# Kernel tuning notes

Hardware: AMD Instinct MI355X
Metric: run time of the kernel (lower is better)

## Reference

```python
import jax, jax.numpy as jnp
import numpy as np

N, E, D, H, L = 100000, 800000, 64, 2, 2
C = D  # out_channels per head
NEG_SLOPE = 0.2


def setup_inputs() -> dict:
    key = jax.random.key(0)
    ks = jax.random.split(key, 10)
    x = jax.random.normal(ks[0], (N, D), dtype=jnp.float32)
    # random edges with no self loops (PyG GATv2 removes then re-adds self loops)
    src = jax.random.randint(ks[1], (E,), 0, N, dtype=jnp.int64)
    off = jax.random.randint(ks[2], (E,), 1, N, dtype=jnp.int64)
    dst = (src + off) % N
    edges_connectivity = jnp.stack([src, dst], axis=0)
    s = 1.0 / np.sqrt(D)
    Wl = jax.random.normal(ks[3], (L, D, H * C), dtype=jnp.float32) * s
    bl = jnp.zeros((L, H * C), dtype=jnp.float32)
    Wr = jax.random.normal(ks[4], (L, D, H * C), dtype=jnp.float32) * s
    br = jnp.zeros((L, H * C), dtype=jnp.float32)
    att = jax.random.normal(ks[5], (L, H, C), dtype=jnp.float32) * s
    bias = jnp.zeros((L, C), dtype=jnp.float32)
    return {"embeded_nodes_features": x, "edges_connectivity": edges_connectivity,
            "Wl": Wl, "bl": bl, "Wr": Wr, "br": br, "att": att, "bias": bias}


def _gatv2_layer(x, src, dst, Wl, bl, Wr, br, att, bias):
    # x: [N, D]; src/dst: [E'] (self loops already appended)
    xl = (x @ Wl + bl).reshape(N, H, C)
    xr = (x @ Wr + br).reshape(N, H, C)
    z = xl[src] + xr[dst]                                  # [E', H, C]
    e = jnp.einsum('ehc,hc->eh', jax.nn.leaky_relu(z, NEG_SLOPE), att)
    m = jax.ops.segment_max(e, dst, num_segments=N)        # [N, H]
    a = jnp.exp(e - m[dst])
    denom = jax.ops.segment_sum(a, dst, num_segments=N)    # [N, H]
    alpha = a / (denom[dst] + 1e-16)
    out = jax.ops.segment_sum(alpha[:, :, None] * xl[src], dst, num_segments=N)
    return out.mean(axis=1) + bias                         # concat=False -> mean over heads


def reference(embeded_nodes_features, edges_connectivity, Wl, bl, Wr, br, att, bias):
    loop = jnp.arange(N, dtype=edges_connectivity.dtype)
    src = jnp.concatenate([edges_connectivity[0], loop])
    dst = jnp.concatenate([edges_connectivity[1], loop])
    x = embeded_nodes_features  # dropout p=0 -> no-op
    for i in range(L):
        x = _gatv2_layer(x, src, dst, Wl[i], bl[i], Wr[i], br[i], att[i], bias[i])
        if i < L - 1:
            x = jax.nn.gelu(x)
    return x
```

## Files before the change

kernel.cpp:

```cpp
#include <hip/hip_runtime.h>
#include <math.h>

#define N_NODES 100000
#define N_EDGES 800000
#define D_IN    64
#define HC      128
#define CAP     48

#define GEMM_BLOCKS 1563
#define FUSED_BLOCKS (3 * GEMM_BLOCKS)

typedef short bf16x8 __attribute__((ext_vector_type(8)));
typedef float f32x4  __attribute__((ext_vector_type(4)));

__device__ __forceinline__ float gelu_f(float x) {
    float x3 = x * x * x;
    float y  = 0.7978845608028654f * (x + 0.044715f * x3);
    float t = 1.0f - 2.0f / (__expf(2.0f * y) + 1.0f);
    return 0.5f * x * (1.0f + t);
}

__device__ __forceinline__ float red16(float x) {
    x += __int_as_float(__builtin_amdgcn_mov_dpp(__float_as_int(x), 0x128, 0xF, 0xF, true));
    x += __int_as_float(__builtin_amdgcn_mov_dpp(__float_as_int(x), 0x124, 0xF, 0xF, true));
    x += __int_as_float(__builtin_amdgcn_mov_dpp(__float_as_int(x), 0x122, 0xF, 0xF, true));
    x += __int_as_float(__builtin_amdgcn_mov_dpp(__float_as_int(x), 0x121, 0xF, 0xF, true));
    return x;
}

__device__ __forceinline__ void bf16split(float x, unsigned short& h, unsigned short& l) {
    unsigned b  = __float_as_uint(x);
    unsigned hb = (b + 0x7FFFu + ((b >> 16) & 1u)) & 0xFFFF0000u;
    h = (unsigned short)(hb >> 16);
    float lo = x - __uint_as_float(hb);
    unsigned c = __float_as_uint(lo);
    l = (unsigned short)((c + 0x7FFFu + ((c >> 16) & 1u)) >> 16);
}

__global__ __launch_bounds__(256) void wprep_kernel(
    const float* __restrict__ Wl, const float* __restrict__ Wr,
    unsigned short* __restrict__ WBh, unsigned short* __restrict__ WBlo) {
    int g = blockIdx.x * 256 + threadIdx.x;
    int layer = g >> 14;
    int rem   = g & 16383;
    int j    = rem & 7;
    int idx  = rem >> 3;
    int lane = idx & 63;
    int kh   = (idx >> 6) & 1;
    int nt   = (idx >> 7) & 3;
    int w    = (idx >> 9) & 3;
    int col  = w * 64 + nt * 16 + (lane & 15);
    int k    = kh * 32 + (lane >> 4) * 8 + j;
    const float* W = (col < 128) ? Wl : Wr;
    float x = W[layer * 8192 + k * HC + (col & 127)];
    unsigned short h, l;
    bf16split(x, h, l);
    WBh[g] = h; WBlo[g] = l;
}

__global__ __launch_bounds__(256, 4) void gemm_scatter_kernel(
    const float* __restrict__ X,
    const unsigned short* __restrict__ WBh, const unsigned short* __restrict__ WBlo,
    const float* __restrict__ bl, const float* __restrict__ br,
    float* __restrict__ XL, float* __restrict__ XR,
    const int* __restrict__ edges, int* __restrict__ cnt, int* __restrict__ tbl,
    int fused) {
    __shared__ union SMem {
        struct { unsigned short XH[64 * 64]; unsigned short XLo[64 * 64]; } st;
        float CS[32 * 268];
    } sm;

    const int t = threadIdx.x;
    int gid;
    if (fused) {
        const int g = blockIdx.x / 3, r = blockIdx.x % 3;
        if (r != 2) {
            const int e = (2 * g + r) * 256 + t;
            if (e < N_EDGES) {
                int s = edges[e];
                int d = edges[N_EDGES + e];
                int slot = atomicAdd(&cnt[d], 1);
                if (slot < CAP) tbl[d * CAP + slot] = s;
            }
            return;
        }
        gid = g;
    } else {
        gid = blockIdx.x;
    }
    const int n0 = gid * 64;

    #pragma unroll
    for (int p = 0; p < 4; ++p) {
        int f   = p * 256 + t;
        int row = f >> 4, q = f & 15;
        int gn  = n0 + row;
        float4 v = make_float4(0.0f, 0.0f, 0.0f, 0.0f);
        if (gn < N_NODES) v = *(const float4*)(X + (size_t)gn * D_IN + 4 * q);
        ushort4 h, l;
        bf16split(v.x, h.x, l.x); bf16split(v.y, h.y, l.y);
        bf16split(v.z, h.z, l.z); bf16split(v.w, h.w, l.w);
        int off = row * 64 + ((((q >> 1) ^ (row & 7))) << 3) + ((q & 1) << 2);
        *(ushort4*)&sm.st.XH[off]  = h;
        *(ushort4*)&sm.st.XLo[off] = l;
    }
    __syncthreads();

    const int lane = t & 63;
    const int w    = __builtin_amdgcn_readfirstlane(t >> 6);
    const float* __restrict__ bp = (w < 2) ? bl : br;
    const int cbase = (w & 1) * 64;
    const int lc    = lane & 15;
    const int lq    = lane >> 4;

    f32x4 acc[4][4];
    #pragma unroll
    for (int nt = 0; nt < 4; ++nt) {
        float bv = bp[cbase + nt * 16 + lc];
        #pragma unroll
        for (int mt = 0; mt < 4; ++mt)
            acc[mt][nt] = (f32x4){bv, bv, bv, bv};
    }

    #pragma unroll
    for (int kh = 0; kh < 2; ++kh) {
        bf16x8 Bh[4], Bl[4];
        #pragma unroll
        for (int nt = 0; nt < 4; ++nt) {
            int a = (((w * 4 + nt) * 2 + kh) * 64 + lane) * 8;
            Bh[nt] = *(const bf16x8*)(WBh + a);
            Bl[nt] = *(const bf16x8*)(WBlo + a);
        }
        #pragma unroll
        for (int mt = 0; mt < 4; ++mt) {
            int row = mt * 16 + lc;
            int aoff = row * 64 + ((((kh << 2) + lq) ^ (row & 7)) << 3);
            bf16x8 Ah = *(const bf16x8*)(sm.st.XH + aoff);
            bf16x8 Al = *(const bf16x8*)(sm.st.XLo + aoff);
            #pragma unroll
            for (int nt = 0; nt < 4; ++nt)
                acc[mt][nt] = __builtin_amdgcn_mfma_f32_16x16x32_bf16(Ah, Bh[nt], acc[mt][nt], 0, 0, 0);
            #pragma unroll
            for (int nt = 0; nt < 4; ++nt)
                acc[mt][nt] = __builtin_amdgcn_mfma_f32_16x16x32_bf16(Al, Bh[nt], acc[mt][nt], 0, 0, 0);
            #pragma unroll
            for (int nt = 0; nt < 4; ++nt)
                acc[mt][nt] = __builtin_amdgcn_mfma_f32_16x16x32_bf16(Ah, Bl[nt], acc[mt][nt], 0, 0, 0);
        }
    }

    #pragma unroll
    for (int c = 0; c < 2; ++c) {
        __syncthreads();
        #pragma unroll
        for (int mt2 = 0; mt2 < 2; ++mt2) {
            int mt = 2 * c + mt2;
            #pragma unroll
            for (int nt = 0; nt < 4; ++nt)
                #pragma unroll
                for (int r = 0; r < 4; ++r)
                    sm.CS[(mt2 * 16 + (lq << 2) + r) * 268 + w * 64 + nt * 16 + lc]
                        = acc[mt][nt][r];
        }
        __syncthreads();
        #pragma unroll
        for (int i = 0; i < 8; ++i) {
            int lr = i * 4 + w;
            int n  = n0 + c * 32 + lr;
            if (n < N_NODES) {
                float4 v4 = *(const float4*)&sm.CS[lr * 268 + 4 * lane];
                float* o = ((lane < 32) ? XL : XR) + (size_t)n * HC + (lane & 31) * 4;
                *(float4*)o = v4;
            }
        }
    }
}

__global__ __launch_bounds__(256) void aggregate_kernel(
    const float* __restrict__ XL, const float* __restrict__ XR,
    const int* __restrict__ cnt, const int* __restrict__ tbl,
    const float* __restrict__ att, const float* __restrict__ bias,
    float* __restrict__ Y, int applyGelu) {
    const int wv   = (blockIdx.x * blockDim.x + threadIdx.x) >> 6;
    const int lane = threadIdx.x & 63;
    const int v    = 2 * wv + (lane >> 5);
    if (v >= N_NODES) return;
    const int li = lane & 15;
    const int hc = ((lane >> 4) & 1) * 64 + 4 * li;
    const int selbase = lane & 32;

    const float4 araw = *(const float4*)(att + hc);
    float4 a06, a04;
    a06.x = araw.x * 0.865617024f; a06.y = araw.y * 0.865617024f;
    a06.z = araw.z * 0.865617024f; a06.w = araw.w * 0.865617024f;
    a04.x = araw.x * 0.577078016f; a04.y = araw.y * 0.577078016f;
    a04.z = araw.z * 0.577078016f; a04.w = araw.w * 0.577078016f;
    const float4 xr4 = *(const float4*)(XR + (size_t)v * HC + hc);
    const float4 xl4 = *(const float4*)(XL + (size_t)v * HC + hc);

#define SCORE4(Z0, Z1, Z2, Z3, OUT)                                          \
    {                                                                        \
        float pa = (Z0) * a06.x;                                             \
        float pb = fabsf(Z0) * a04.x;                                        \
        pa = fmaf((Z1), a06.y, pa); pb = fmaf(fabsf(Z1), a04.y, pb);         \
        pa = fmaf((Z2), a06.z, pa); pb = fmaf(fabsf(Z2), a04.z, pb);         \
        pa = fmaf((Z3), a06.w, pa); pb = fmaf(fabsf(Z3), a04.w, pb);         \
        OUT = pa + pb;                                                       \
    }

    float z0 = xl4.x + xr4.x, z1 = xl4.y + xr4.y;
    float z2 = xl4.z + xr4.z, z3 = xl4.w + xr4.w;
    float p;
    SCORE4(z0, z1, z2, z3, p)
    const float m0 = red16(p);

    float s = 1.0f;
    float ax = xl4.x, ay = xl4.y, az = xl4.z, aw = xl4.w;

    int deg = cnt[v];
    if (deg > CAP) deg = CAP;
    const int slot = lane & 31;
    int u_l = (slot < deg) ? tbl[v * CAP + slot] : 0;

    int dmax = deg;
    { int d2 = __shfl_xor(deg, 32); dmax = d2 > dmax ? d2 : dmax; }

    const float* __restrict__ XLh = XL + hc;

    float4 x0 = make_float4(0,0,0,0), x1 = x0, x2 = x0;
    if (dmax > 0) { int u = __shfl(u_l, 0 + selbase); x0 = *(const float4*)(XLh + (size_t)u * HC); }
    if (dmax > 1) { int u = __shfl(u_l, 1 + selbase); x1 = *(const float4*)(XLh + (size_t)u * HC); }
    if (dmax > 2) { int u = __shfl(u_l, 2 + selbase); x2 = *(const float4*)(XLh + (size_t)u * HC); }

    for (int i = 0; i < dmax; ++i) {
        float4 xc = x0; x0 = x1; x1 = x2;
        int pf = i + 3;
        if (pf < dmax) {
            int u = (pf < 32) ? __shfl(u_l, pf + selbase) : tbl[v * CAP + pf];
            x2 = *(const float4*)(XLh + (size_t)u * HC);
        }
        z0 = xc.x + xr4.x; z1 = xc.y + xr4.y;
        z2 = xc.z + xr4.z; z3 = xc.w + xr4.w;
        SCORE4(z0, z1, z2, z3, p)
        p = red16(p);
        if (i >= deg) p = -1e30f;
        float w = exp2f(p - m0);
        s += w;
        ax = fmaf(w, xc.x, ax); ay = fmaf(w, xc.y, ay);
        az = fmaf(w, xc.z, az); aw = fmaf(w, xc.w, aw);
    }
#undef SCORE4

    float inv = 1.0f / (s + 1e-16f);
    ax *= inv; ay *= inv; az *= inv; aw *= inv;

    ax += __shfl_xor(ax, 16); ay += __shfl_xor(ay, 16);
    az += __shfl_xor(az, 16); aw += __shfl_xor(aw, 16);
    ax *= 0.5f; ay *= 0.5f; az *= 0.5f; aw *= 0.5f;

    if ((lane & 31) < 16) {
        const float4 b4 = *(const float4*)(bias + 4 * li);
        ax += b4.x; ay += b4.y; az += b4.z; aw += b4.w;
        if (applyGelu) { ax = gelu_f(ax); ay = gelu_f(ay); az = gelu_f(az); aw = gelu_f(aw); }
        *(float4*)(Y + (size_t)v * 64 + 4 * li) = make_float4(ax, ay, az, aw);
    }
}

extern "C" void kernel_launch(void* const* d_in, const int* in_sizes, int n_in,
                              void* d_out, int out_size, void* d_ws, size_t ws_size,
                              hipStream_t stream) {
    const float* X     = (const float*)d_in[0];
    const int*   edges = (const int*)d_in[1];
    const float* Wl    = (const float*)d_in[2];
    const float* bl    = (const float*)d_in[3];
    const float* Wr    = (const float*)d_in[4];
    const float* br    = (const float*)d_in[5];
    const float* att   = (const float*)d_in[6];
    const float* bias  = (const float*)d_in[7];

    char* ws = (char*)d_ws;
    float* XLb = (float*)ws;
    float* XRb = (float*)(ws + (size_t)N_NODES * HC * 4);
    float* Yb  = (float*)(ws + (size_t)N_NODES * HC * 8);
    int*   cnt = (int*)(ws + (size_t)N_NODES * HC * 8 + (size_t)N_NODES * 64 * 4);
    int*   tbl = cnt + N_NODES;
    unsigned short* WBh  = (unsigned short*)(tbl + (size_t)N_NODES * CAP);
    unsigned short* WBlo = WBh + 32768;

    hipMemsetAsync(cnt, 0, N_NODES * sizeof(int), stream);
    wprep_kernel<<<128, 256, 0, stream>>>(Wl, Wr, WBh, WBlo);

    const int agg_grid = ((N_NODES + 1) / 2 * 64 + 255) / 256;

    gemm_scatter_kernel<<<FUSED_BLOCKS, 256, 0, stream>>>(
        X, WBh, WBlo, bl, br, XLb, XRb, edges, cnt, tbl, 1);
    aggregate_kernel<<<agg_grid, 256, 0, stream>>>(XLb, XRb, cnt, tbl, att, bias, Yb, 1);
    gemm_scatter_kernel<<<GEMM_BLOCKS, 256, 0, stream>>>(
        Yb, WBh + 16384, WBlo + 16384, bl + 128, br + 128, XLb, XRb, edges, cnt, tbl, 0);
    aggregate_kernel<<<agg_grid, 256, 0, stream>>>(XLb, XRb, cnt, tbl, att + 128, bias + 64,
                                                   (float*)d_out, 0);
}
```

Baseline: 308.8 us.

## Load neighbor indices as int4 and deepen gather pipeline with unrolled quads

Replaces the shuffle-broadcast of neighbor indices with direct per-lane int4 loads of the adjacency table, and restructures the aggregation loop into a fully unrolled 12-quad schedule that prefetches gathers two quads (8 neighbors) ahead. Masking moves to a weight-zeroing select, and indices are clamped with a bitmask so speculative loads stay in bounds. The goal is more memory-level parallelism on the random XL gathers, at the cost of many more registers (dq[12][4] float4s), which may reduce occupancy or cause spills.

```diff
diff --git a/kernel.cpp b/kernel.cpp
--- a/kernel.cpp
+++ b/kernel.cpp
@@ -187,16 +187,23 @@
     if (v >= N_NODES) return;
     const int li = lane & 15;
     const int hc = ((lane >> 4) & 1) * 64 + 4 * li;
-    const int selbase = lane & 32;
+
+    int deg = cnt[v];
+    const int* __restrict__ tv = tbl + v * CAP;
+    int4 ic[12];
+    ic[0] = *(const int4*)(tv);
+    ic[1] = *(const int4*)(tv + 4);
+    ic[2] = *(const int4*)(tv + 8);
+    ic[3] = *(const int4*)(tv + 12);
 
     const float4 araw = *(const float4*)(att + hc);
+    const float4 xr4  = *(const float4*)(XR + (size_t)v * HC + hc);
+    const float4 xl4  = *(const float4*)(XL + (size_t)v * HC + hc);
     float4 a06, a04;
     a06.x = araw.x * 0.865617024f; a06.y = araw.y * 0.865617024f;
     a06.z = araw.z * 0.865617024f; a06.w = araw.w * 0.865617024f;
     a04.x = araw.x * 0.577078016f; a04.y = araw.y * 0.577078016f;
     a04.z = araw.z * 0.577078016f; a04.w = araw.w * 0.577078016f;
-    const float4 xr4 = *(const float4*)(XR + (size_t)v * HC + hc);
-    const float4 xl4 = *(const float4*)(XL + (size_t)v * HC + hc);
 
 #define SCORE4(Z0, Z1, Z2, Z3, OUT)                                          \
     {                                                                        \
@@ -217,38 +224,57 @@
     float s = 1.0f;
     float ax = xl4.x, ay = xl4.y, az = xl4.z, aw = xl4.w;
 
-    int deg = cnt[v];
     if (deg > CAP) deg = CAP;
-    const int slot = lane & 31;
-    int u_l = (slot < deg) ? tbl[v * CAP + slot] : 0;
-
     int dmax = deg;
     { int d2 = __shfl_xor(deg, 32); dmax = d2 > dmax ? d2 : dmax; }
 
     const float* __restrict__ XLh = XL + hc;
-
-    float4 x0 = make_float4(0,0,0,0), x1 = x0, x2 = x0;
-    if (dmax > 0) { int u = __shfl(u_l, 0 + selbase); x0 = *(const float4*)(XLh + (size_t)u * HC); }
-    if (dmax > 1) { int u = __shfl(u_l, 1 + selbase); x1 = *(const float4*)(XLh + (size_t)u * HC); }
-    if (dmax > 2) { int u = __shfl(u_l, 2 + selbase); x2 = *(const float4*)(XLh + (size_t)u * HC); }
-
-    for (int i = 0; i < dmax; ++i) {
-        float4 xc = x0; x0 = x1; x1 = x2;
-        int pf = i + 3;
-        if (pf < dmax) {
-            int u = (pf < 32) ? __shfl(u_l, pf + selbase) : tbl[v * CAP + pf];
-            x2 = *(const float4*)(XLh + (size_t)u * HC);
-        }
-        z0 = xc.x + xr4.x; z1 = xc.y + xr4.y;
-        z2 = xc.z + xr4.z; z3 = xc.w + xr4.w;
-        SCORE4(z0, z1, z2, z3, p)
-        p = red16(p);
-        if (i >= deg) p = -1e30f;
-        float w = exp2f(p - m0);
-        s += w;
-        ax = fmaf(w, xc.x, ax); ay = fmaf(w, xc.y, ay);
-        az = fmaf(w, xc.z, az); aw = fmaf(w, xc.w, aw);
-    }
+    float4 dq[12][4];
+
+#define GLD(U) (*(const float4*)(XLh + (size_t)((U) & 131071) * HC))
+#define LOADQ(q)                                                             \
+    {                                                                        \
+        int4 uu = ic[(q)];                                                   \
+        float4 t0 = make_float4(0,0,0,0), t1 = t0, t2 = t0, t3 = t0;         \
+        if (4*(q) + 0 < deg) t0 = GLD(uu.x);                                 \
+        if (4*(q) + 1 < deg) t1 = GLD(uu.y);                                 \
+        if (4*(q) + 2 < deg) t2 = GLD(uu.z);                                 \
+        if (4*(q) + 3 < deg) t3 = GLD(uu.w);                                 \
+        dq[(q)][0] = t0; dq[(q)][1] = t1; dq[(q)][2] = t2; dq[(q)][3] = t3;  \
+    }
+
+#define BODY(T, J)                                                           \
+    {                                                                        \
+        float4 xc = dq[(T)][(J)];                                            \
+        float y0 = xc.x + xr4.x, y1 = xc.y + xr4.y;                          \
+        float y2 = xc.z + xr4.z, y3 = xc.w + xr4.w;                          \
+        float pe;                                                            \
+        SCORE4(y0, y1, y2, y3, pe)                                           \
+        pe = red16(pe);                                                      \
+        float w = exp2f(pe - m0);                                            \
+        w = (4*(T) + (J) < deg) ? w : 0.0f;                                  \
+        s += w;                                                              \
+        ax = fmaf(w, xc.x, ax); ay = fmaf(w, xc.y, ay);                      \
+        az = fmaf(w, xc.z, az); aw = fmaf(w, xc.w, aw);                      \
+    }
+
+    if (dmax > 0) {
+        LOADQ(0)
+        if (dmax > 4) LOADQ(1)
+        #pragma unroll
+        for (int t = 0; t < 12; ++t) {
+            if (4 * t < dmax) {
+                if (t + 4 < 12 && 4 * (t + 4) < dmax + 16)
+                    ic[t + 4] = *(const int4*)(tv + 4 * (t + 4));
+                if (t + 2 < 12 && 4 * (t + 2) < dmax)
+                    LOADQ(t + 2)
+                BODY(t, 0) BODY(t, 1) BODY(t, 2) BODY(t, 3)
+            }
+        }
+    }
+#undef BODY
+#undef LOADQ
+#undef GLD
 #undef SCORE4
 
     float inv = 1.0f / (s + 1e-16f);
```

Result: slower. 328.6 us (+6.4%).
